# Kernel optimization log

Hardware: AMD Instinct MI355X
Metric: run time of the kernel (lower is better)

Reference implementation:

```python
import jax, jax.numpy as jnp
import numpy as np

B, S, HID = 2, 2048, 2048
N_HEADS, N_KV, HEAD_DIM = 8, 1, 256
ROPE_THETA = 10000.0
NEG = -1e9


def setup_inputs() -> dict:
    key = jax.random.key(0)
    ks = jax.random.split(key, 6)
    hidden_states = jax.random.normal(ks[0], (B, S, HID), dtype=jnp.float32)
    position_ids = jnp.broadcast_to(jnp.arange(S, dtype=jnp.int32)[None, :], (B, S))
    causal = jnp.tril(jnp.ones((S, S), dtype=bool))
    attention_mask = jnp.where(causal, 0.0, NEG).astype(jnp.float32)[None, None]
    attention_mask = jnp.broadcast_to(attention_mask, (B, 1, S, S))
    sc = 0.02
    Wq = jax.random.normal(ks[1], (N_HEADS * HEAD_DIM, HID), dtype=jnp.float32) * sc
    Wk = jax.random.normal(ks[2], (N_KV * HEAD_DIM, HID), dtype=jnp.float32) * sc
    Wv = jax.random.normal(ks[3], (N_KV * HEAD_DIM, HID), dtype=jnp.float32) * sc
    Wo = jax.random.normal(ks[4], (HID, N_HEADS * HEAD_DIM), dtype=jnp.float32) * sc
    return {"hidden_states": hidden_states, "position_ids": position_ids,
            "attention_mask": attention_mask, "Wq": Wq, "Wk": Wk, "Wv": Wv, "Wo": Wo}


def _rotate_half(x):
    x1, x2 = jnp.split(x, 2, axis=-1)
    return jnp.concatenate((-x2, x1), axis=-1)


def _rope_cos_sin(position_ids, head_dim, dtype):
    inv_freq = 1.0 / (ROPE_THETA ** (jnp.arange(0, head_dim, 2, dtype=jnp.float32) / head_dim))
    freqs = position_ids.astype(jnp.float32)[:, :, None] * inv_freq[None, None, :]  # [B,S,D/2]
    emb = jnp.concatenate((freqs, freqs), axis=-1)  # [B,S,D]
    return jnp.cos(emb).astype(dtype), jnp.sin(emb).astype(dtype)


def reference(hidden_states, position_ids, attention_mask, Wq, Wk, Wv, Wo):
    b, s, _ = hidden_states.shape
    d = HEAD_DIM
    rep = N_HEADS // N_KV
    q = (hidden_states @ Wq.T).reshape(b, s, N_HEADS, d).transpose(0, 2, 1, 3)  # [B,H,S,D]
    k = (hidden_states @ Wk.T).reshape(b, s, N_KV, d).transpose(0, 2, 1, 3)    # [B,KV,S,D]
    v = (hidden_states @ Wv.T).reshape(b, s, N_KV, d).transpose(0, 2, 1, 3)
    cos, sin = _rope_cos_sin(position_ids, d, hidden_states.dtype)
    cos, sin = cos[:, None], sin[:, None]  # broadcast over heads
    q = q * cos + _rotate_half(q) * sin
    k = k * cos + _rotate_half(k) * sin
    # GQA: group queries per kv head, no materialized repeat
    qg = q.reshape(b, N_KV, rep, s, d)
    scores = jnp.einsum('bgrqd,bgkd->bgrqk', qg, k) / jnp.sqrt(jnp.float32(d)).astype(q.dtype)
    scores = scores.reshape(b, N_HEADS, s, s) + attention_mask
    probs = jax.nn.softmax(scores.astype(jnp.float32), axis=-1).astype(q.dtype)
    out = jnp.einsum('bgrqk,bgkd->bgrqd', probs.reshape(b, N_KV, rep, s, s), v)
    out = out.reshape(b, N_HEADS, s, d).transpose(0, 2, 1, 3).reshape(b, s, N_HEADS * d)
    return out @ Wo.T
```

## Files before the change

kernel.cpp:

```cpp
#include <hip/hip_runtime.h>
#include <hip/hip_bf16.h>

typedef __bf16 bf16x8 __attribute__((ext_vector_type(8)));
typedef float  f32x4  __attribute__((ext_vector_type(4)));

#define BATCH 2
#define SEQ   2048
#define HID   2048
#define NH    8
#define DH    256
#define LQ    2560
#define ROWS  (BATCH*SEQ)
#define KVB   32

__device__ __forceinline__ void gld16(const void* g, void* l) {
    __builtin_amdgcn_global_load_lds(
        (__attribute__((address_space(1))) void*)(g),
        (__attribute__((address_space(3))) void*)(l), 16, 0, 0);
}

__device__ __forceinline__ unsigned pack2bf(float a, float b) {
    union { __bf16 h[2]; unsigned u; } x;
    x.h[0] = (__bf16)a; x.h[1] = (__bf16)b;
    return x.u;
}

__global__ void cvt_f32_bf16(const float* __restrict__ src, __bf16* __restrict__ dst, int n4) {
    int i = blockIdx.x * blockDim.x + threadIdx.x;
    if (i < n4) {
        float4 v = ((const float4*)src)[i];
        __bf16 o[4];
        o[0] = (__bf16)v.x; o[1] = (__bf16)v.y; o[2] = (__bf16)v.z; o[3] = (__bf16)v.w;
        ((uint2*)dst)[i] = *(uint2*)o;
    }
}

template<typename CT>
__global__ __launch_bounds__(256)
void gemm_bt(const __bf16* __restrict__ A, const __bf16* __restrict__ B,
             CT* __restrict__ C, int M, int N, int K) {
    __shared__ __bf16 sA[128 * 32];
    __shared__ __bf16 sB[128 * 32];
    const int tid  = threadIdx.x;
    const int lane = tid & 63;
    const int wid  = tid >> 6;
    const int row0 = blockIdx.y * 128;
    const int col0 = blockIdx.x * 128;
    const int wr = (wid >> 1) * 64;
    const int wc = (wid & 1) * 64;

    const int sr0 = tid >> 2, sc0 = (tid & 3) * 8;
    const __bf16* Ag0 = A + (size_t)(row0 + sr0) * K + sc0;
    const __bf16* Ag1 = Ag0 + (size_t)64 * K;
    const __bf16* Bg0 = B + (size_t)(col0 + sr0) * K + sc0;
    const __bf16* Bg1 = Bg0 + (size_t)64 * K;
    __bf16* lA0 = &sA[wid * 512];
    __bf16* lA1 = &sA[2048 + wid * 512];
    __bf16* lB0 = &sB[wid * 512];
    __bf16* lB1 = &sB[2048 + wid * 512];

    f32x4 acc[4][4];
#pragma unroll
    for (int m = 0; m < 4; ++m)
#pragma unroll
        for (int n = 0; n < 4; ++n) acc[m][n] = (f32x4)0.f;

    for (int k0 = 0; k0 < K; k0 += 32) {
        gld16(Ag0 + k0, lA0);
        gld16(Ag1 + k0, lA1);
        gld16(Bg0 + k0, lB0);
        gld16(Bg1 + k0, lB1);
        __syncthreads();
        bf16x8 af[4], bfr[4];
#pragma unroll
        for (int m = 0; m < 4; ++m)
            af[m] = *(const bf16x8*)&sA[(wr + m * 16 + (lane & 15)) * 32 + (lane >> 4) * 8];
#pragma unroll
        for (int n = 0; n < 4; ++n)
            bfr[n] = *(const bf16x8*)&sB[(wc + n * 16 + (lane & 15)) * 32 + (lane >> 4) * 8];
#pragma unroll
        for (int m = 0; m < 4; ++m)
#pragma unroll
            for (int n = 0; n < 4; ++n)
                acc[m][n] = __builtin_amdgcn_mfma_f32_16x16x32_bf16(af[m], bfr[n], acc[m][n], 0, 0, 0);
        __syncthreads();
    }
#pragma unroll
    for (int m = 0; m < 4; ++m)
#pragma unroll
        for (int n = 0; n < 4; ++n)
#pragma unroll
            for (int r = 0; r < 4; ++r) {
                int row = row0 + wr + m * 16 + (lane >> 4) * 4 + r;
                int col = col0 + wc + n * 16 + (lane & 15);
                C[(size_t)row * N + col] = (CT)acc[m][n][r];
            }
}

__global__ void rope_kernel(__bf16* __restrict__ QKV, const int* __restrict__ pid) {
    const int row = blockIdx.x;
    const int h   = blockIdx.y;
    const int j   = threadIdx.x;
    const float pos = (float)pid[row];
    const float freq = exp2f((float)j * (-13.287712379549449f / 128.0f));
    const float ang = pos * freq;
    float sn, cs;
    sincosf(ang, &sn, &cs);
    const float sc = (h < 8) ? 0.0625f : 1.0f;
    __bf16* p = QKV + (size_t)row * LQ + h * 256 + j;
    float x1 = (float)p[0], x2 = (float)p[128];
    p[0]   = (__bf16)((x1 * cs - x2 * sn) * sc);
    p[128] = (__bf16)((x2 * cs + x1 * sn) * sc);
}

__global__ __launch_bounds__(256)
void transpose_v(const __bf16* __restrict__ QKV, __bf16* __restrict__ Vt) {
    __shared__ __bf16 t[32][33];
    const int b  = blockIdx.z;
    const int s0 = blockIdx.x * 32;
    const int d0 = blockIdx.y * 32;
    const int c  = threadIdx.x & 31;
    const int r8 = threadIdx.x >> 5;
#pragma unroll
    for (int i = 0; i < 4; ++i) {
        int row = r8 + i * 8;
        t[row][c] = QKV[(size_t)(b * SEQ + s0 + row) * LQ + 2304 + d0 + c];
    }
    __syncthreads();
#pragma unroll
    for (int i = 0; i < 4; ++i) {
        int row = r8 + i * 8;
        Vt[((size_t)b * 256 + d0 + row) * SEQ + s0 + c] = t[c][row];
    }
}

__global__ __launch_bounds__(512, 2)
void attn_fwd4(const __bf16* __restrict__ QKV, const __bf16* __restrict__ Vt,
               __bf16* __restrict__ O) {
    __shared__ __bf16 Kt[2][KVB * 256];
    __shared__ __bf16 Vs[2][256 * KVB];

    const int tid  = threadIdx.x;
    const int lane = tid & 63;
    const int wid  = tid >> 6;
    const int lc   = lane & 15;
    const int l4   = lane >> 4;

    const int bid = blockIdx.x;
    const int b   = bid >> 7;
    const int qt  = bid & 127;
    const int q0  = qt * 16;
    const int nt  = (qt >> 1) + 1;
    const int h   = wid;

    const char* QKVb = (const char*)(QKV + (size_t)(b * SEQ) * LQ);
    const char* Kg   = QKVb + 2048 * 2;
    const char* Vg   = (const char*)(Vt + (size_t)b * DH * SEQ);

    const int kr0   = wid * 4 + (lane >> 5);
    const int kcolb = (lane & 31) * 16;
    const int vd0   = wid * 32 + (lane >> 2);
    const int vcol0 = (lane & 3) * 16;
    const int vrsw  = ((lc >> 1) & 3) << 4;

#define STAGE(B_, KV0) do {                                                         \
    _Pragma("unroll")                                                               \
    for (int i_ = 0; i_ < 2; ++i_) {                                                \
        int r_ = kr0 + i_ * 2;                                                      \
        gld16(Kg + (size_t)((KV0) + r_) * (LQ * 2) + (kcolb ^ ((r_ & 7) << 4)),     \
              (char*)&Kt[B_][0] + (wid * 2 + i_) * 1024);                           \
    }                                                                               \
    _Pragma("unroll")                                                               \
    for (int i_ = 0; i_ < 2; ++i_) {                                                \
        int d_ = vd0 + i_ * 16;                                                     \
        gld16(Vg + (size_t)d_ * (SEQ * 2) + (KV0) * 2 + (vcol0 ^ (((d_ >> 1) & 3) << 4)), \
              (char*)&Vs[B_][0] + (wid * 2 + i_) * 1024);                           \
    }                                                                               \
} while (0)

    const char* Qp = QKVb + (size_t)(q0 + lc) * (LQ * 2) + h * 512 + l4 * 16;
    bf16x8 qf[8];
#pragma unroll
    for (int kc = 0; kc < 8; ++kc) qf[kc] = *(const bf16x8*)(Qp + kc * 64);

    f32x4 oacc[16];
#pragma unroll
    for (int i = 0; i < 16; ++i) oacc[i] = (f32x4)0.f;
    float mrow = -1e30f, lrow = 0.f;
    const int qrow = q0 + lc;

    STAGE(0, 0);

    int buf = 0;
    for (int t = 0; t < nt; ++t) {
        __syncthreads();
        const int kv0 = t * KVB;
        if (t + 1 < nt) STAGE(buf ^ 1, kv0 + KVB);

        f32x4 sacc[2];
        sacc[0] = (f32x4)0.f; sacc[1] = (f32x4)0.f;
        const char* Kl = (const char*)&Kt[buf][0];
        __builtin_amdgcn_s_setprio(1);
#pragma unroll
        for (int kc = 0; kc < 8; ++kc) {
#pragma unroll
            for (int ct = 0; ct < 2; ++ct) {
                const int rr = ct * 16 + lc;
                bf16x8 kf = *(const bf16x8*)(Kl + rr * 512 +
                                             (((kc << 6) | (l4 << 4)) ^ ((rr & 7) << 4)));
                sacc[ct] = __builtin_amdgcn_mfma_f32_16x16x32_bf16(kf, qf[kc], sacc[ct], 0, 0, 0);
            }
        }
        __builtin_amdgcn_s_setprio(0);

        const bool lastt = (t == nt - 1);
        float tm = -1e30f;
#pragma unroll
        for (int ct = 0; ct < 2; ++ct)
#pragma unroll
            for (int r = 0; r < 4; ++r) {
                float s = sacc[ct][r];
                if (lastt) {
                    int kv = kv0 + ct * 16 + l4 * 4 + r;
                    if (kv > qrow) s = -1e30f;
                }
                sacc[ct][r] = s;
                tm = fmaxf(tm, s);
            }
        tm = fmaxf(tm, __shfl_xor(tm, 16, 64));
        tm = fmaxf(tm, __shfl_xor(tm, 32, 64));
        if (!__all(tm <= mrow + 8.f)) {
            const float mnew  = fmaxf(mrow, tm);
            const float alpha = __expf(mrow - mnew);
            mrow = mnew;
            lrow *= alpha;
#pragma unroll
            for (int dt = 0; dt < 16; ++dt) {
                oacc[dt][0] *= alpha; oacc[dt][1] *= alpha;
                oacc[dt][2] *= alpha; oacc[dt][3] *= alpha;
            }
        }
        float p0[4], p1[4], ps = 0.f;
#pragma unroll
        for (int r = 0; r < 4; ++r) { p0[r] = __expf(sacc[0][r] - mrow); ps += p0[r]; }
#pragma unroll
        for (int r = 0; r < 4; ++r) { p1[r] = __expf(sacc[1][r] - mrow); ps += p1[r]; }
        ps += __shfl_xor(ps, 16, 64);
        ps += __shfl_xor(ps, 32, 64);
        lrow += ps;

        unsigned pkA0 = pack2bf(p0[0], p0[1]), pkA1 = pack2bf(p0[2], p0[3]);
        unsigned pkB0 = pack2bf(p1[0], p1[1]), pkB1 = pack2bf(p1[2], p1[3]);
        const int sl0 = lc + 16 * ((2 * l4) & 3);
        const int sl1 = lc + 16 * ((2 * l4 + 1) & 3);
        unsigned a0 = __shfl(pkA0, sl0, 64), a1 = __shfl(pkA1, sl0, 64);
        unsigned b0 = __shfl(pkB0, sl0, 64), b1 = __shfl(pkB1, sl0, 64);
        unsigned c0 = __shfl(pkA0, sl1, 64), c1 = __shfl(pkA1, sl1, 64);
        unsigned d0 = __shfl(pkB0, sl1, 64), d1 = __shfl(pkB1, sl1, 64);
        const bool hi = (l4 >= 2);
        union { unsigned u[4]; bf16x8 v; } pb;
        pb.u[0] = hi ? b0 : a0;
        pb.u[1] = hi ? b1 : a1;
        pb.u[2] = hi ? d0 : c0;
        pb.u[3] = hi ? d1 : c1;

        const char* Vl = (const char*)&Vs[buf][0];
        __builtin_amdgcn_s_setprio(1);
#pragma unroll
        for (int dt = 0; dt < 16; ++dt) {
            bf16x8 vf = *(const bf16x8*)(Vl + (dt * 16 + lc) * 64 + ((l4 << 4) ^ vrsw));
            oacc[dt] = __builtin_amdgcn_mfma_f32_16x16x32_bf16(vf, pb.v, oacc[dt], 0, 0, 0);
        }
        __builtin_amdgcn_s_setprio(0);
        buf ^= 1;
    }

    const float inv = 1.f / lrow;
    char* Op = (char*)O + ((size_t)(b * SEQ + q0 + lc) * HID + h * 256 + l4 * 4) * 2;
#pragma unroll
    for (int dt = 0; dt < 16; ++dt) {
        __bf16 o4[4];
        o4[0] = (__bf16)(oacc[dt][0] * inv);
        o4[1] = (__bf16)(oacc[dt][1] * inv);
        o4[2] = (__bf16)(oacc[dt][2] * inv);
        o4[3] = (__bf16)(oacc[dt][3] * inv);
        *(uint2*)(Op + dt * 32) = *(uint2*)o4;
    }
#undef STAGE
}

extern "C" void kernel_launch(void* const* d_in, const int* in_sizes, int n_in,
                              void* d_out, int out_size, void* d_ws, size_t ws_size,
                              hipStream_t stream) {
    const float* hs  = (const float*)d_in[0];
    const int*   pid = (const int*)d_in[1];
    const float* Wq  = (const float*)d_in[3];
    const float* Wk  = (const float*)d_in[4];
    const float* Wv  = (const float*)d_in[5];
    const float* Wo  = (const float*)d_in[6];
    float* out = (float*)d_out;

    char* ws = (char*)d_ws;
    __bf16* Xb   = (__bf16*)ws;                       ws += (size_t)ROWS * HID * 2;
    __bf16* Wqkv = (__bf16*)ws;                       ws += (size_t)LQ * HID * 2;
    __bf16* Wob  = (__bf16*)ws;                       ws += (size_t)HID * HID * 2;
    __bf16* QKV  = (__bf16*)ws;                       ws += (size_t)ROWS * LQ * 2;
    __bf16* Vt   = (__bf16*)ws;                       ws += (size_t)BATCH * DH * SEQ * 2;
    __bf16* Oat  = Xb;

    cvt_f32_bf16<<<(ROWS * HID / 4 + 255) / 256, 256, 0, stream>>>(hs, Xb, ROWS * HID / 4);
    cvt_f32_bf16<<<(HID * HID / 4 + 255) / 256, 256, 0, stream>>>(Wq, Wqkv, HID * HID / 4);
    cvt_f32_bf16<<<(DH * HID / 4 + 255) / 256, 256, 0, stream>>>(Wk, Wqkv + (size_t)2048 * HID, DH * HID / 4);
    cvt_f32_bf16<<<(DH * HID / 4 + 255) / 256, 256, 0, stream>>>(Wv, Wqkv + (size_t)2304 * HID, DH * HID / 4);
    cvt_f32_bf16<<<(HID * HID / 4 + 255) / 256, 256, 0, stream>>>(Wo, Wob, HID * HID / 4);

    gemm_bt<__bf16><<<dim3(LQ / 128, ROWS / 128), 256, 0, stream>>>(Xb, Wqkv, QKV, ROWS, LQ, HID);

    rope_kernel<<<dim3(ROWS, 9), 128, 0, stream>>>(QKV, pid);

    transpose_v<<<dim3(SEQ / 32, DH / 32, BATCH), 256, 0, stream>>>(QKV, Vt);

    attn_fwd4<<<dim3(256), 512, 0, stream>>>(QKV, Vt, Oat);

    gemm_bt<float><<<dim3(HID / 128, ROWS / 128), 256, 0, stream>>>(Oat, Wob, out, ROWS, HID, HID);
}
```

Measured before the change: 393.5 us.

## Balance causal attention with paired query tiles and split-KV merge

Each attention block now handles two query tiles (c and 127-c) so causal work is balanced across blocks. The KV range of each tile is split in half between two blocks, and the partial unnormalised outputs plus max/sum statistics go to separate buffers. A new merge kernel combines them. The P fragment shuffle is also replaced by an LDS round trip. This removes the load imbalance and tail of the triangular workload, at the cost of an extra kernel, extra workspace traffic and bf16 rounding of the unnormalised partials.

Result: faster. 360.6 us (-8.4%).

```diff
diff --git a/kernel.cpp b/kernel.cpp
--- a/kernel.cpp
+++ b/kernel.cpp
@@ -135,10 +135,12 @@
 }
 
 __global__ __launch_bounds__(512, 2)
-void attn_fwd4(const __bf16* __restrict__ QKV, const __bf16* __restrict__ Vt,
-               __bf16* __restrict__ O) {
+void attn_fwd5(const __bf16* __restrict__ QKV, const __bf16* __restrict__ Vt,
+               __bf16* __restrict__ A0, __bf16* __restrict__ A1,
+               float2* __restrict__ ML) {
     __shared__ __bf16 Kt[2][KVB * 256];
     __shared__ __bf16 Vs[2][256 * KVB];
+    __shared__ char   Pl[8][16 * 80];
 
     const int tid  = threadIdx.x;
     const int lane = tid & 63;
@@ -148,9 +150,8 @@
 
     const int bid = blockIdx.x;
     const int b   = bid >> 7;
-    const int qt  = bid & 127;
-    const int q0  = qt * 16;
-    const int nt  = (qt >> 1) + 1;
+    const int pg  = bid & 63;
+    const int kvh = (bid >> 6) & 1;
     const int h   = wid;
 
     const char* QKVb = (const char*)(QKV + (size_t)(b * SEQ) * LQ);
@@ -162,6 +163,7 @@
     const int vd0   = wid * 32 + (lane >> 2);
     const int vcol0 = (lane & 3) * 16;
     const int vrsw  = ((lc >> 1) & 3) << 4;
+    char* Pw = &Pl[wid][0];
 
 #define STAGE(B_, KV0) do {                                                         \
     _Pragma("unroll")                                                               \
@@ -178,115 +180,144 @@
     }                                                                               \
 } while (0)
 
-    const char* Qp = QKVb + (size_t)(q0 + lc) * (LQ * 2) + h * 512 + l4 * 16;
-    bf16x8 qf[8];
-#pragma unroll
-    for (int kc = 0; kc < 8; ++kc) qf[kc] = *(const bf16x8*)(Qp + kc * 64);
-
-    f32x4 oacc[16];
-#pragma unroll
-    for (int i = 0; i < 16; ++i) oacc[i] = (f32x4)0.f;
-    float mrow = -1e30f, lrow = 0.f;
-    const int qrow = q0 + lc;
-
-    STAGE(0, 0);
-
-    int buf = 0;
-    for (int t = 0; t < nt; ++t) {
+    for (int seg = 0; seg < 2; ++seg) {
+        const int c    = seg ? (127 - pg) : pg;
+        const int ntc  = (c >> 1) + 1;
+        const int t0   = kvh ? (ntc >> 1) : 0;
+        const int t1   = kvh ? ntc : (ntc >> 1);
+        const int q0   = c * 16;
+        const int qrow = q0 + lc;
+
+        const char* Qp = QKVb + (size_t)(q0 + lc) * (LQ * 2) + h * 512 + l4 * 16;
+        bf16x8 qf[8];
+#pragma unroll
+        for (int kc = 0; kc < 8; ++kc) qf[kc] = *(const bf16x8*)(Qp + kc * 64);
+
+        f32x4 oacc[16];
+#pragma unroll
+        for (int i = 0; i < 16; ++i) oacc[i] = (f32x4)0.f;
+        float mrow = -1e30f, lrow = 0.f;
+
         __syncthreads();
-        const int kv0 = t * KVB;
-        if (t + 1 < nt) STAGE(buf ^ 1, kv0 + KVB);
-
-        f32x4 sacc[2];
-        sacc[0] = (f32x4)0.f; sacc[1] = (f32x4)0.f;
-        const char* Kl = (const char*)&Kt[buf][0];
-        __builtin_amdgcn_s_setprio(1);
-#pragma unroll
-        for (int kc = 0; kc < 8; ++kc) {
-#pragma unroll
-            for (int ct = 0; ct < 2; ++ct) {
-                const int rr = ct * 16 + lc;
-                bf16x8 kf = *(const bf16x8*)(Kl + rr * 512 +
-                                             (((kc << 6) | (l4 << 4)) ^ ((rr & 7) << 4)));
-                sacc[ct] = __builtin_amdgcn_mfma_f32_16x16x32_bf16(kf, qf[kc], sacc[ct], 0, 0, 0);
+        if (t0 < t1) {
+            STAGE(0, t0 * KVB);
+            int buf = 0;
+            for (int t = t0; t < t1; ++t) {
+                __syncthreads();
+                const int kv0 = t * KVB;
+                if (t + 1 < t1) STAGE(buf ^ 1, kv0 + KVB);
+
+                f32x4 sacc[2];
+                sacc[0] = (f32x4)0.f; sacc[1] = (f32x4)0.f;
+                const char* Kl = (const char*)&Kt[buf][0];
+                __builtin_amdgcn_s_setprio(1);
+#pragma unroll
+                for (int kc = 0; kc < 8; ++kc) {
+#pragma unroll
+                    for (int ct = 0; ct < 2; ++ct) {
+                        const int rr = ct * 16 + lc;
+                        bf16x8 kf = *(const bf16x8*)(Kl + rr * 512 +
+                                                     (((kc << 6) | (l4 << 4)) ^ ((rr & 7) << 4)));
+                        sacc[ct] = __builtin_amdgcn_mfma_f32_16x16x32_bf16(kf, qf[kc], sacc[ct], 0, 0, 0);
+                    }
+                }
+                __builtin_amdgcn_s_setprio(0);
+
+                const bool lastt = (t == ntc - 1);
+                float tm = -1e30f;
+#pragma unroll
+                for (int ct = 0; ct < 2; ++ct)
+#pragma unroll
+                    for (int r = 0; r < 4; ++r) {
+                        float s = sacc[ct][r];
+                        if (lastt) {
+                            int kv = kv0 + ct * 16 + l4 * 4 + r;
+                            if (kv > qrow) s = -1e30f;
+                        }
+                        sacc[ct][r] = s;
+                        tm = fmaxf(tm, s);
+                    }
+                tm = fmaxf(tm, __shfl_xor(tm, 16, 64));
+                tm = fmaxf(tm, __shfl_xor(tm, 32, 64));
+                if (!__all(tm <= mrow + 8.f)) {
+                    const float mnew  = fmaxf(mrow, tm);
+                    const float alpha = __expf(mrow - mnew);
+                    mrow = mnew;
+                    lrow *= alpha;
+#pragma unroll
+                    for (int dt = 0; dt < 16; ++dt) {
+                        oacc[dt][0] *= alpha; oacc[dt][1] *= alpha;
+                        oacc[dt][2] *= alpha; oacc[dt][3] *= alpha;
+                    }
+                }
+                float p0[4], p1[4], ps = 0.f;
+#pragma unroll
+                for (int r = 0; r < 4; ++r) { p0[r] = __expf(sacc[0][r] - mrow); ps += p0[r]; }
+#pragma unroll
+                for (int r = 0; r < 4; ++r) { p1[r] = __expf(sacc[1][r] - mrow); ps += p1[r]; }
+                ps += __shfl_xor(ps, 16, 64);
+                ps += __shfl_xor(ps, 32, 64);
+                lrow += ps;
+
+                *(uint2*)(Pw + lc * 80 + l4 * 8) =
+                    make_uint2(pack2bf(p0[0], p0[1]), pack2bf(p0[2], p0[3]));
+                *(uint2*)(Pw + lc * 80 + 32 + l4 * 8) =
+                    make_uint2(pack2bf(p1[0], p1[1]), pack2bf(p1[2], p1[3]));
+                asm volatile("s_waitcnt lgkmcnt(0)" ::: "memory");
+                __builtin_amdgcn_sched_barrier(0);
+                bf16x8 pb = *(const bf16x8*)(Pw + lc * 80 + l4 * 16);
+
+                const char* Vl = (const char*)&Vs[buf][0];
+                __builtin_amdgcn_s_setprio(1);
+#pragma unroll
+                for (int dt = 0; dt < 16; ++dt) {
+                    bf16x8 vf = *(const bf16x8*)(Vl + (dt * 16 + lc) * 64 + ((l4 << 4) ^ vrsw));
+                    oacc[dt] = __builtin_amdgcn_mfma_f32_16x16x32_bf16(vf, pb, oacc[dt], 0, 0, 0);
+                }
+                __builtin_amdgcn_s_setprio(0);
+                buf ^= 1;
             }
         }
-        __builtin_amdgcn_s_setprio(0);
-
-        const bool lastt = (t == nt - 1);
-        float tm = -1e30f;
-#pragma unroll
-        for (int ct = 0; ct < 2; ++ct)
-#pragma unroll
-            for (int r = 0; r < 4; ++r) {
-                float s = sacc[ct][r];
-                if (lastt) {
-                    int kv = kv0 + ct * 16 + l4 * 4 + r;
-                    if (kv > qrow) s = -1e30f;
-                }
-                sacc[ct][r] = s;
-                tm = fmaxf(tm, s);
-            }
-        tm = fmaxf(tm, __shfl_xor(tm, 16, 64));
-        tm = fmaxf(tm, __shfl_xor(tm, 32, 64));
-        if (!__all(tm <= mrow + 8.f)) {
-            const float mnew  = fmaxf(mrow, tm);
-            const float alpha = __expf(mrow - mnew);
-            mrow = mnew;
-            lrow *= alpha;
-#pragma unroll
-            for (int dt = 0; dt < 16; ++dt) {
-                oacc[dt][0] *= alpha; oacc[dt][1] *= alpha;
-                oacc[dt][2] *= alpha; oacc[dt][3] *= alpha;
-            }
+
+        __bf16* dst = kvh ? A1 : A0;
+        char* Op = (char*)dst + ((size_t)(b * SEQ + q0 + lc) * HID + h * 256 + l4 * 4) * 2;
+#pragma unroll
+        for (int dt = 0; dt < 16; ++dt) {
+            __bf16 o4[4];
+            o4[0] = (__bf16)oacc[dt][0];
+            o4[1] = (__bf16)oacc[dt][1];
+            o4[2] = (__bf16)oacc[dt][2];
+            o4[3] = (__bf16)oacc[dt][3];
+            *(uint2*)(Op + dt * 32) = *(uint2*)o4;
         }
-        float p0[4], p1[4], ps = 0.f;
-#pragma unroll
-        for (int r = 0; r < 4; ++r) { p0[r] = __expf(sacc[0][r] - mrow); ps += p0[r]; }
-#pragma unroll
-        for (int r = 0; r < 4; ++r) { p1[r] = __expf(sacc[1][r] - mrow); ps += p1[r]; }
-        ps += __shfl_xor(ps, 16, 64);
-        ps += __shfl_xor(ps, 32, 64);
-        lrow += ps;
-
-        unsigned pkA0 = pack2bf(p0[0], p0[1]), pkA1 = pack2bf(p0[2], p0[3]);
-        unsigned pkB0 = pack2bf(p1[0], p1[1]), pkB1 = pack2bf(p1[2], p1[3]);
-        const int sl0 = lc + 16 * ((2 * l4) & 3);
-        const int sl1 = lc + 16 * ((2 * l4 + 1) & 3);
-        unsigned a0 = __shfl(pkA0, sl0, 64), a1 = __shfl(pkA1, sl0, 64);
-        unsigned b0 = __shfl(pkB0, sl0, 64), b1 = __shfl(pkB1, sl0, 64);
-        unsigned c0 = __shfl(pkA0, sl1, 64), c1 = __shfl(pkA1, sl1, 64);
-        unsigned d0 = __shfl(pkB0, sl1, 64), d1 = __shfl(pkB1, sl1, 64);
-        const bool hi = (l4 >= 2);
-        union { unsigned u[4]; bf16x8 v; } pb;
-        pb.u[0] = hi ? b0 : a0;
-        pb.u[1] = hi ? b1 : a1;
-        pb.u[2] = hi ? d0 : c0;
-        pb.u[3] = hi ? d1 : c1;
-
-        const char* Vl = (const char*)&Vs[buf][0];
-        __builtin_amdgcn_s_setprio(1);
-#pragma unroll
-        for (int dt = 0; dt < 16; ++dt) {
-            bf16x8 vf = *(const bf16x8*)(Vl + (dt * 16 + lc) * 64 + ((l4 << 4) ^ vrsw));
-            oacc[dt] = __builtin_amdgcn_mfma_f32_16x16x32_bf16(vf, pb.v, oacc[dt], 0, 0, 0);
-        }
-        __builtin_amdgcn_s_setprio(0);
-        buf ^= 1;
-    }
-
-    const float inv = 1.f / lrow;
-    char* Op = (char*)O + ((size_t)(b * SEQ + q0 + lc) * HID + h * 256 + l4 * 4) * 2;
-#pragma unroll
-    for (int dt = 0; dt < 16; ++dt) {
-        __bf16 o4[4];
-        o4[0] = (__bf16)(oacc[dt][0] * inv);
-        o4[1] = (__bf16)(oacc[dt][1] * inv);
-        o4[2] = (__bf16)(oacc[dt][2] * inv);
-        o4[3] = (__bf16)(oacc[dt][3] * inv);
-        *(uint2*)(Op + dt * 32) = *(uint2*)o4;
+        if (l4 == 0)
+            ML[(size_t)kvh * ROWS * NH + (size_t)(b * SEQ + q0 + lc) * NH + h] =
+                make_float2(mrow, lrow);
     }
 #undef STAGE
+}
+
+__global__ __launch_bounds__(256)
+void merge_attn(__bf16* __restrict__ A0, const __bf16* __restrict__ A1,
+                const float2* __restrict__ ML) {
+    const int idx = blockIdx.x * 256 + threadIdx.x;
+    const int r = idx >> 8;
+    const int g = idx & 255;
+    const int h = g >> 5;
+    const float2 ml0 = ML[(size_t)r * NH + h];
+    const float2 ml1 = ML[(size_t)ROWS * NH + (size_t)r * NH + h];
+    const float M  = fmaxf(ml0.x, ml1.x);
+    float w0 = __expf(ml0.x - M), w1 = __expf(ml1.x - M);
+    const float inv = 1.0f / (ml0.y * w0 + ml1.y * w1);
+    w0 *= inv; w1 *= inv;
+    const size_t off = (size_t)r * HID + (size_t)g * 8;
+    bf16x8 a0 = *(const bf16x8*)(A0 + off);
+    bf16x8 a1 = *(const bf16x8*)(A1 + off);
+    bf16x8 o;
+#pragma unroll
+    for (int j = 0; j < 8; ++j)
+        o[j] = (__bf16)((float)a0[j] * w0 + (float)a1[j] * w1);
+    *(bf16x8*)(A0 + off) = o;
 }
 
 extern "C" void kernel_launch(void* const* d_in, const int* in_sizes, int n_in,
@@ -301,12 +332,14 @@
     float* out = (float*)d_out;
 
     char* ws = (char*)d_ws;
-    __bf16* Xb   = (__bf16*)ws;                       ws += (size_t)ROWS * HID * 2;
-    __bf16* Wqkv = (__bf16*)ws;                       ws += (size_t)LQ * HID * 2;
-    __bf16* Wob  = (__bf16*)ws;                       ws += (size_t)HID * HID * 2;
-    __bf16* QKV  = (__bf16*)ws;                       ws += (size_t)ROWS * LQ * 2;
-    __bf16* Vt   = (__bf16*)ws;                       ws += (size_t)BATCH * DH * SEQ * 2;
-    __bf16* Oat  = Xb;
+    __bf16* Xb    = (__bf16*)ws;                      ws += (size_t)ROWS * HID * 2;
+    __bf16* Wqkv  = (__bf16*)ws;                      ws += (size_t)LQ * HID * 2;
+    __bf16* Wob   = (__bf16*)ws;                      ws += (size_t)HID * HID * 2;
+    __bf16* QKV   = (__bf16*)ws;                      ws += (size_t)ROWS * LQ * 2;
+    __bf16* Vt    = (__bf16*)ws;                      ws += (size_t)BATCH * DH * SEQ * 2;
+    __bf16* Apart = (__bf16*)ws;                      ws += (size_t)ROWS * HID * 2;
+    float2* ML    = (float2*)ws;                      ws += (size_t)2 * ROWS * NH * sizeof(float2);
+    __bf16* Oat   = Xb;
 
     cvt_f32_bf16<<<(ROWS * HID / 4 + 255) / 256, 256, 0, stream>>>(hs, Xb, ROWS * HID / 4);
     cvt_f32_bf16<<<(HID * HID / 4 + 255) / 256, 256, 0, stream>>>(Wq, Wqkv, HID * HID / 4);
@@ -320,7 +353,9 @@
 
     transpose_v<<<dim3(SEQ / 32, DH / 32, BATCH), 256, 0, stream>>>(QKV, Vt);
 
-    attn_fwd4<<<dim3(256), 512, 0, stream>>>(QKV, Vt, Oat);
+    attn_fwd5<<<dim3(256), 512, 0, stream>>>(QKV, Vt, Oat, Apart, ML);
+
+    merge_attn<<<dim3(ROWS * HID / 8 / 256), 256, 0, stream>>>(Oat, Apart, ML);
 
     gemm_bt<float><<<dim3(HID / 128, ROWS / 128), 256, 0, stream>>>(Oat, Wob, out, ROWS, HID, HID);
 }
```
